# Optimization experiments

Hardware: AMD Instinct MI355X
Metric: run time of the kernel (lower is better)

## Reference

```python
import jax, jax.numpy as jnp
import numpy as np

NUM_HEADS = 16
HEAD_SIZE = 64
N_EMBD = 1024


def setup_inputs() -> dict:
    key = jax.random.key(0)
    ks = jax.random.split(key, 6)
    B, T, C = 2, 2048, N_EMBD
    scale = 0.02
    return {
        "x": jax.random.normal(ks[0], (B, T, C), dtype=jnp.float32),
        "Wq": jax.random.normal(ks[1], (C, NUM_HEADS * HEAD_SIZE), dtype=jnp.float32) * scale,
        "Wk": jax.random.normal(ks[2], (C, NUM_HEADS * HEAD_SIZE), dtype=jnp.float32) * scale,
        "Wv": jax.random.normal(ks[3], (C, NUM_HEADS * HEAD_SIZE), dtype=jnp.float32) * scale,
        "Wo": jax.random.normal(ks[4], (NUM_HEADS * HEAD_SIZE, C), dtype=jnp.float32) * scale,
        "bo": jnp.zeros((C,), dtype=jnp.float32),
    }


def reference(x, Wq, Wk, Wv, Wo, bo):
    B, T, C = x.shape
    H, D = NUM_HEADS, HEAD_SIZE
    # QKV projections (no bias), reshape to [B, H, T, D]
    q = (x @ Wq).reshape(B, T, H, D).transpose(0, 2, 1, 3)
    k = (x @ Wk).reshape(B, T, H, D).transpose(0, 2, 1, 3)
    v = (x @ Wv).reshape(B, T, H, D).transpose(0, 2, 1, 3)
    # scaled dot-product scores [B, H, T, T]
    scores = jnp.einsum("bhqd,bhkd->bhqk", q, k) / jnp.sqrt(jnp.float32(D))
    causal = jnp.tril(jnp.ones((T, T), dtype=bool))
    scores = jnp.where(causal, scores, -jnp.inf)
    weights = jax.nn.softmax(scores, axis=-1)  # dropout = identity (eval)
    out = jnp.einsum("bhqk,bhkd->bhqd", weights, v)
    out = out.transpose(0, 2, 1, 3).reshape(B, T, H * D)
    return out @ Wo + bo
```

## Files before the change

kernel.cpp:

```cpp
#include <hip/hip_runtime.h>

typedef __attribute__((ext_vector_type(8))) _Float16 f16x8;
typedef __attribute__((ext_vector_type(4))) _Float16 f16x4;
typedef __attribute__((ext_vector_type(2))) _Float16 f16x2;
typedef __attribute__((ext_vector_type(2))) __fp16   fp16x2_raw;
typedef __attribute__((ext_vector_type(4))) float    f32x4;

#define NUM_HEADS 16
#define HEAD_D 64
#define EMB 1024
#define SEQ 2048
#define BATCH 2
#define MTOT (BATCH * SEQ)

#define QALPHA 0.18033688011112042f

__device__ __forceinline__ f16x2 cvt_pk_f16(float lo, float hi)
{
    fp16x2_raw r = __builtin_amdgcn_cvt_pkrtz(lo, hi);
    return __builtin_bit_cast(f16x2, r);
}

#if defined(__has_builtin)
#if __has_builtin(__builtin_amdgcn_exp2f)
#define HAVE_EXP2 1
#endif
#endif
__device__ __forceinline__ float fast_exp2(float x)
{
#ifdef HAVE_EXP2
    return __builtin_amdgcn_exp2f(x);
#else
    return __expf(x * 0.6931471805599453f);
#endif
}

#if defined(__has_builtin)
#if __has_builtin(__builtin_amdgcn_global_load_lds)
#define HAVE_GLOAD_LDS 1
#endif
#endif

__device__ __forceinline__ void stage16(const void* g, void* ldsWaveBase, int lane)
{
#ifdef HAVE_GLOAD_LDS
    __builtin_amdgcn_global_load_lds(
        (const __attribute__((address_space(1))) void*)g,
        (__attribute__((address_space(3))) void*)ldsWaveBase, 16, 0, 0);
    (void)lane;
#else
    *(f16x8*)((char*)ldsWaveBase + lane * 16) = *(const f16x8*)g;
#endif
}

__global__ __launch_bounds__(256) void prep_all(
    const float* __restrict__ x,
    const float* __restrict__ Wq, const float* __restrict__ Wk,
    const float* __restrict__ Wv, const float* __restrict__ Wo,
    _Float16* __restrict__ xh, _Float16* __restrict__ Wt,
    _Float16* __restrict__ Wto)
{
    const int z = blockIdx.z;
    if (z == 4) {
        int base = ((blockIdx.y * 32 + blockIdx.x) * 256 + threadIdx.x) * 2;
        #pragma unroll
        for (int t = 0; t < 2; ++t) {
            int i = base + t;
            float4 a = ((const float4*)x)[i * 2];
            float4 b = ((const float4*)x)[i * 2 + 1];
            f16x8 o;
            o[0] = (_Float16)a.x; o[1] = (_Float16)a.y;
            o[2] = (_Float16)a.z; o[3] = (_Float16)a.w;
            o[4] = (_Float16)b.x; o[5] = (_Float16)b.y;
            o[6] = (_Float16)b.z; o[7] = (_Float16)b.w;
            ((f16x8*)xh)[i] = o;
        }
        return;
    }
    const float* W = z == 0 ? Wq : (z == 1 ? Wk : (z == 2 ? Wv : Wo));
    _Float16* D = (z == 3) ? Wto : (Wt + (size_t)z * EMB * EMB);
    __shared__ float tile[32][33];
    const int tx = threadIdx.x & 31, ty = threadIdx.x >> 5;
    const int n0 = blockIdx.x * 32, k0 = blockIdx.y * 32;
    #pragma unroll
    for (int j = 0; j < 4; ++j)
        tile[ty + j * 8][tx] = W[(size_t)(k0 + ty + j * 8) * EMB + n0 + tx];
    __syncthreads();
    #pragma unroll
    for (int j = 0; j < 4; ++j)
        D[(size_t)(n0 + ty + j * 8) * EMB + k0 + tx] =
            (_Float16)tile[tx][ty + j * 8];
}

__global__ __launch_bounds__(256) void gemm_qkv(
    const _Float16* __restrict__ A, const _Float16* __restrict__ Bt,
    _Float16* __restrict__ Qh, _Float16* __restrict__ Kh,
    _Float16* __restrict__ VhT)
{
    __shared__ __align__(16) _Float16 As[128 * 32];
    __shared__ __align__(16) _Float16 Bs[128 * 32];

    const int tid = threadIdx.x;
    const int w = tid >> 6, lane = tid & 63;
    const int l15 = lane & 15, g4 = lane >> 4;
    const int wm = w >> 1, wn = w & 1;

    const int wg = blockIdx.y * gridDim.x + blockIdx.x;
    const int t  = (wg & 7) * 96 + (wg >> 3);
    const int bx = t >> 5, by = t & 31;
    const int row0 = by * 128, col0 = bx * 128;

    f32x4 acc[4][4];
    #pragma unroll
    for (int mt = 0; mt < 4; ++mt)
        #pragma unroll
        for (int nt = 0; nt < 4; ++nt)
            acc[mt][nt] = (f32x4){0.f, 0.f, 0.f, 0.f};

    for (int k0 = 0; k0 < EMB; k0 += 32) {
        __syncthreads();
        #pragma unroll
        for (int i = 0; i < 2; ++i) {
            int c = (i << 8) + tid;
            int row = c >> 2, u = c & 3;
            stage16(&A[(size_t)(row0 + row) * EMB + k0 + (u << 3)],
                    (char*)As + (i << 12) + (w << 10), lane);
            stage16(&Bt[(size_t)(col0 + row) * EMB + k0 + (u << 3)],
                    (char*)Bs + (i << 12) + (w << 10), lane);
        }
        __syncthreads();

        f16x8 af[4], bf[4];
        #pragma unroll
        for (int mt = 0; mt < 4; ++mt)
            af[mt] = *(const f16x8*)((const char*)As +
                     ((wm << 6) + (mt << 4) + l15) * 64 + (g4 << 4));
        #pragma unroll
        for (int nt = 0; nt < 4; ++nt)
            bf[nt] = *(const f16x8*)((const char*)Bs +
                     ((wn << 6) + (nt << 4) + l15) * 64 + (g4 << 4));
        #pragma unroll
        for (int mt = 0; mt < 4; ++mt)
            #pragma unroll
            for (int nt = 0; nt < 4; ++nt)
                acc[mt][nt] = __builtin_amdgcn_mfma_f32_16x16x32_f16(
                    af[mt], bf[nt], acc[mt][nt], 0, 0, 0);
    }

    #pragma unroll
    for (int mt = 0; mt < 4; ++mt) {
        int m = row0 + (wm << 6) + (mt << 4) + (g4 << 2);
        #pragma unroll
        for (int nt = 0; nt < 4; ++nt) {
            int gcol = col0 + (wn << 6) + (nt << 4) + l15;
            int proj = gcol >> 10, pc = gcol & 1023;
            int h = pc >> 6, d = pc & 63;
            int b = m >> 11, tt = m & 2047;
            int bh = b * NUM_HEADS + h;
            if (proj == 2) {
                f16x4 v4;
                v4[0] = (_Float16)acc[mt][nt][0];
                v4[1] = (_Float16)acc[mt][nt][1];
                v4[2] = (_Float16)acc[mt][nt][2];
                v4[3] = (_Float16)acc[mt][nt][3];
                *(f16x4*)&VhT[((size_t)bh * HEAD_D + d) * SEQ + tt] = v4;
            } else {
                _Float16* dst = proj == 0 ? Qh : Kh;
                float alpha = proj == 0 ? QALPHA : 1.0f;
                #pragma unroll
                for (int r = 0; r < 4; ++r)
                    dst[((size_t)bh * SEQ + tt + r) * HEAD_D + d] =
                        (_Float16)(acc[mt][nt][r] * alpha);
            }
        }
    }
}

__global__ __launch_bounds__(256) void gemm_out(
    const _Float16* __restrict__ A, const _Float16* __restrict__ Bt,
    float* __restrict__ outf, const float* __restrict__ bias)
{
    __shared__ __align__(16) _Float16 As[128 * 32];
    __shared__ __align__(16) _Float16 Bs[64 * 32];

    const int tid = threadIdx.x;
    const int w = tid >> 6, lane = tid & 63;
    const int l15 = lane & 15, g4 = lane >> 4;
    const int wm = w >> 1, wn = w & 1;

    const int wg = blockIdx.y * gridDim.x + blockIdx.x;
    const int t  = (wg & 7) * 64 + (wg >> 3);
    const int bx = t >> 5, by = t & 31;
    const int row0 = by * 128, col0 = bx * 64;

    f32x4 acc[4][2];
    #pragma unroll
    for (int mt = 0; mt < 4; ++mt)
        #pragma unroll
        for (int nt = 0; nt < 2; ++nt)
            acc[mt][nt] = (f32x4){0.f, 0.f, 0.f, 0.f};

    for (int k0 = 0; k0 < EMB; k0 += 32) {
        __syncthreads();
        #pragma unroll
        for (int i = 0; i < 2; ++i) {
            int c = (i << 8) + tid;
            int row = c >> 2, u = c & 3;
            stage16(&A[(size_t)(row0 + row) * EMB + k0 + (u << 3)],
                    (char*)As + (i << 12) + (w << 10), lane);
        }
        {
            int row = tid >> 2, u = tid & 3;
            stage16(&Bt[(size_t)(col0 + row) * EMB + k0 + (u << 3)],
                    (char*)Bs + (w << 10), lane);
        }
        __syncthreads();

        f16x8 af[4], bf[2];
        #pragma unroll
        for (int mt = 0; mt < 4; ++mt)
            af[mt] = *(const f16x8*)((const char*)As +
                     ((wm << 6) + (mt << 4) + l15) * 64 + (g4 << 4));
        #pragma unroll
        for (int nt = 0; nt < 2; ++nt)
            bf[nt] = *(const f16x8*)((const char*)Bs +
                     ((wn << 5) + (nt << 4) + l15) * 64 + (g4 << 4));
        #pragma unroll
        for (int mt = 0; mt < 4; ++mt)
            #pragma unroll
            for (int nt = 0; nt < 2; ++nt)
                acc[mt][nt] = __builtin_amdgcn_mfma_f32_16x16x32_f16(
                    af[mt], bf[nt], acc[mt][nt], 0, 0, 0);
    }

    #pragma unroll
    for (int mt = 0; mt < 4; ++mt) {
        int m = row0 + (wm << 6) + (mt << 4) + (g4 << 2);
        #pragma unroll
        for (int nt = 0; nt < 2; ++nt) {
            int gcol = col0 + (wn << 5) + (nt << 4) + l15;
            float bz = bias[gcol];
            #pragma unroll
            for (int r = 0; r < 4; ++r)
                outf[(size_t)(m + r) * EMB + gcol] = acc[mt][nt][r] + bz;
        }
    }
}

__device__ __forceinline__ void stage_kv_tile(
    const _Float16* __restrict__ KhB, const _Float16* __restrict__ VtB,
    int kv0, char* __restrict__ KsBuf, char* __restrict__ VtBuf,
    int w, int lane)
{
    #pragma unroll
    for (int i = 0; i < 2; ++i) {
        int c = (i << 8) + (w << 6) + lane;
        int row = c >> 3, u = c & 7;
        int us = u ^ (row & 7);
        stage16(&KhB[(size_t)(kv0 + row) * HEAD_D + (us << 3)],
                KsBuf + (i << 12) + (w << 10), lane);
        stage16(&VtB[(size_t)row * SEQ + kv0 + (us << 3)],
                VtBuf + (i << 12) + (w << 10), lane);
    }
}

__device__ __forceinline__ void attn_tile(
    const char* __restrict__ KsC, const char* __restrict__ VtC,
    char* __restrict__ pwv,
    f16x8 qf0, f16x8 qf1, f32x4 (&acc)[4], float& m, float& l,
    bool diag, int qrel, int l15, int g)
{
    f32x4 st[4];
    #pragma unroll
    for (int nt = 0; nt < 4; ++nt) {
        int kvl = (nt << 4) + l15;
        f16x8 kf0 = *(const f16x8*)&KsC[kvl * 128 + (((g << 4)) ^ ((kvl & 7) << 4))];
        f16x8 kf1 = *(const f16x8*)&KsC[kvl * 128 + ((64 + (g << 4)) ^ ((kvl & 7) << 4))];
        f32x4 z = (f32x4){0.f, 0.f, 0.f, 0.f};
        z = __builtin_amdgcn_mfma_f32_16x16x32_f16(kf0, qf0, z, 0, 0, 0);
        z = __builtin_amdgcn_mfma_f32_16x16x32_f16(kf1, qf1, z, 0, 0, 0);
        st[nt] = z;
    }
    if (diag) {
        #pragma unroll
        for (int nt = 0; nt < 4; ++nt)
            #pragma unroll
            for (int r = 0; r < 4; ++r)
                if ((nt << 4) + (g << 2) + r > qrel) st[nt][r] = -1e30f;
    }

    float mx;
    {
        float a0 = fmaxf(fmaxf(st[0][0], st[0][1]), fmaxf(st[0][2], st[0][3]));
        float a1 = fmaxf(fmaxf(st[1][0], st[1][1]), fmaxf(st[1][2], st[1][3]));
        float a2 = fmaxf(fmaxf(st[2][0], st[2][1]), fmaxf(st[2][2], st[2][3]));
        float a3 = fmaxf(fmaxf(st[3][0], st[3][1]), fmaxf(st[3][2], st[3][3]));
        mx = fmaxf(fmaxf(a0, a1), fmaxf(a2, a3));
    }

    if (!__all(mx - m <= 8.0f)) {
        float mxr = fmaxf(mx, __shfl_xor(mx, 16));
        mxr = fmaxf(mxr, __shfl_xor(mxr, 32));
        float nm = fmaxf(m, mxr);
        float sc = fast_exp2(m - nm);
        m = nm;
        l *= sc;
        #pragma unroll
        for (int r = 0; r < 4; ++r) {
            float scr = __shfl(sc, (g << 2) + r);
            acc[0][r] *= scr; acc[1][r] *= scr;
            acc[2][r] *= scr; acc[3][r] *= scr;
        }
    }

    float ps = 0.f;
    #pragma unroll
    for (int nt = 0; nt < 4; ++nt)
        #pragma unroll
        for (int r = 0; r < 4; ++r) {
            float p = fast_exp2(st[nt][r] - m);
            st[nt][r] = p;
            ps += p;
        }
    l += ps;

    #pragma unroll
    for (int nt = 0; nt < 4; ++nt)
        #pragma unroll
        for (int rr = 0; rr < 2; ++rr) {
            int kvb = (nt << 4) + (g << 2) + (rr << 1);
            f16x2 pv = cvt_pk_f16(st[nt][rr * 2], st[nt][rr * 2 + 1]);
            *(f16x2*)&pwv[l15 * 128 + ((kvb << 1) ^ ((l15 & 7) << 4))] = pv;
        }
    f16x8 pa0 = *(const f16x8*)&pwv[l15 * 128 + (((g << 4)) ^ ((l15 & 7) << 4))];
    f16x8 pa1 = *(const f16x8*)&pwv[l15 * 128 + ((64 + (g << 4)) ^ ((l15 & 7) << 4))];

    #pragma unroll
    for (int dn = 0; dn < 4; ++dn) {
        int d = (dn << 4) + l15;
        f16x8 vf0 = *(const f16x8*)&VtC[d * 128 + (((g << 4)) ^ ((d & 7) << 4))];
        f16x8 vf1 = *(const f16x8*)&VtC[d * 128 + ((64 + (g << 4)) ^ ((d & 7) << 4))];
        acc[dn] = __builtin_amdgcn_mfma_f32_16x16x32_f16(pa0, vf0, acc[dn], 0, 0, 0);
        acc[dn] = __builtin_amdgcn_mfma_f32_16x16x32_f16(pa1, vf1, acc[dn], 0, 0, 0);
    }
}

__global__ __launch_bounds__(256) void attn_mfma(
    const _Float16* __restrict__ Qh, const _Float16* __restrict__ Kh,
    const _Float16* __restrict__ VhT, _Float16* __restrict__ O)
{
    __shared__ char lds[48 * 1024];

    const int qtA = blockIdx.x;
    const int qtB = (SEQ / 64 - 1) - qtA;
    const int bh = blockIdx.y;
    const int q0A = qtA << 6, q0B = qtB << 6;
    const int tid = threadIdx.x;
    const int w = tid >> 6, lane = tid & 63;
    const int l15 = lane & 15, g = lane >> 4;

    const _Float16* KhB = Kh  + (size_t)bh * SEQ * HEAD_D;
    const _Float16* VtB = VhT + (size_t)bh * HEAD_D * SEQ;
    const size_t headbase = (size_t)bh * SEQ * HEAD_D;

    const int qrowA = q0A + (w << 4) + l15;
    const int qrowB = q0B + (w << 4) + l15;
    f16x8 qfA0 = *(const f16x8*)&Qh[headbase + (size_t)qrowA * HEAD_D + (g << 3)];
    f16x8 qfA1 = *(const f16x8*)&Qh[headbase + (size_t)qrowA * HEAD_D + 32 + (g << 3)];
    f16x8 qfB0 = *(const f16x8*)&Qh[headbase + (size_t)qrowB * HEAD_D + (g << 3)];
    f16x8 qfB1 = *(const f16x8*)&Qh[headbase + (size_t)qrowB * HEAD_D + 32 + (g << 3)];

    f32x4 accA[4], accB[4];
    #pragma unroll
    for (int dn = 0; dn < 4; ++dn) {
        accA[dn] = (f32x4){0.f, 0.f, 0.f, 0.f};
        accB[dn] = (f32x4){0.f, 0.f, 0.f, 0.f};
    }
    float mA = -1e30f, lA = 0.f, mB = -1e30f, lB = 0.f;

    stage_kv_tile(KhB, VtB, 0, lds, lds + 16384, w, lane);
    __syncthreads();

    char* pwvA = lds + 32768 + (w << 11);
    char* pwvB = lds + 40960 + (w << 11);

    int cur = 0;
    for (int kt = 0; kt <= qtB; ++kt) {
        if (kt < qtB)
            stage_kv_tile(KhB, VtB, (kt + 1) << 6,
                          lds + ((cur ^ 1) << 13),
                          lds + 16384 + ((cur ^ 1) << 13), w, lane);

        const char* KsC = lds + (cur << 13);
        const char* VtC = lds + 16384 + (cur << 13);
        const int qrel = (w << 4) + l15;

        if (kt <= qtA) {
            attn_tile(KsC, VtC, pwvA, qfA0, qfA1, accA, mA, lA,
                      kt == qtA, qrel, l15, g);
            attn_tile(KsC, VtC, pwvB, qfB0, qfB1, accB, mB, lB,
                      false, qrel, l15, g);
        } else {
            attn_tile(KsC, VtC, pwvB, qfB0, qfB1, accB, mB, lB,
                      kt == qtB, qrel, l15, g);
        }

        __syncthreads();
        cur ^= 1;
    }

    lA += __shfl_xor(lA, 16); lA += __shfl_xor(lA, 32);
    lB += __shfl_xor(lB, 16); lB += __shfl_xor(lB, 32);
    const int b = bh >> 4, h = bh & 15;
    const float rlA = 1.f / lA, rlB = 1.f / lB;
    #pragma unroll
    for (int r = 0; r < 4; ++r) {
        float invA = __shfl(rlA, (g << 2) + r);
        float invB = __shfl(rlB, (g << 2) + r);
        int tokA = (b << 11) + q0A + (w << 4) + (g << 2) + r;
        int tokB = (b << 11) + q0B + (w << 4) + (g << 2) + r;
        #pragma unroll
        for (int dn = 0; dn < 4; ++dn) {
            O[(size_t)tokA * EMB + (h << 6) + (dn << 4) + l15] =
                (_Float16)(accA[dn][r] * invA);
            O[(size_t)tokB * EMB + (h << 6) + (dn << 4) + l15] =
                (_Float16)(accB[dn][r] * invB);
        }
    }
}

extern "C" void kernel_launch(void* const* d_in, const int* in_sizes, int n_in,
                              void* d_out, int out_size, void* d_ws, size_t ws_size,
                              hipStream_t stream)
{
    const float* x  = (const float*)d_in[0];
    const float* Wq = (const float*)d_in[1];
    const float* Wk = (const float*)d_in[2];
    const float* Wv = (const float*)d_in[3];
    const float* Wo = (const float*)d_in[4];
    const float* bo = (const float*)d_in[5];
    float* out = (float*)d_out;

    const size_t ME = (size_t)MTOT * EMB;
    const size_t WE = (size_t)EMB * EMB;
    const size_t need = (5 * ME + 4 * WE) * sizeof(_Float16);
    if (ws_size < need) return;

    _Float16* xh  = (_Float16*)d_ws;
    _Float16* Wt  = xh + ME;
    _Float16* Wto = Wt + 3 * WE;
    _Float16* Qh  = Wto + WE;
    _Float16* Kh  = Qh + ME;
    _Float16* VhT = Kh + ME;
    _Float16* Ow  = VhT + ME;

    prep_all<<<dim3(EMB / 32, EMB / 32, 5), 256, 0, stream>>>(
        x, Wq, Wk, Wv, Wo, xh, Wt, Wto);

    gemm_qkv<<<dim3(3 * EMB / 128, MTOT / 128), 256, 0, stream>>>(
        xh, Wt, Qh, Kh, VhT);

    attn_mfma<<<dim3(SEQ / 128, BATCH * NUM_HEADS), 256, 0, stream>>>(Qh, Kh, VhT, Ow);

    gemm_out<<<dim3(EMB / 64, MTOT / 128), 256, 0, stream>>>(
        Ow, Wto, out, bo);
}
```

Measured before the change: 116.7 us.

## Deepen KV prefetch to a 4-slot ring and pair tiles in B-only phase

Expands the KV LDS staging from double-buffering to a 4-slot ring with a prefetch distance of two tiles. The loop is split into three phases: a joint A/B phase, a single-tile transition step, and a B-only phase. The B-only phase uses a new attn_tile2 that computes scores for two KV tiles and does one online-softmax max/rescale per pair, halving barriers and rescale overhead there. The cost is LDS growing from 48 KB to 80 KB per block, which cuts how many blocks fit per CU. The launch_bounds hint of 4 blocks per CU cannot be met with that LDS footprint.

```diff
diff --git a/kernel.cpp b/kernel.cpp
--- a/kernel.cpp
+++ b/kernel.cpp
@@ -345,11 +345,108 @@
     }
 }
 
-__global__ __launch_bounds__(256) void attn_mfma(
+__device__ __forceinline__ void attn_tile2(
+    const char* __restrict__ Ks0, const char* __restrict__ Vt0,
+    const char* __restrict__ Ks1, const char* __restrict__ Vt1,
+    char* __restrict__ pwv,
+    f16x8 qf0, f16x8 qf1, f32x4 (&acc)[4], float& m, float& l,
+    bool diag1, int qrel, int l15, int g)
+{
+    f32x4 st[8];
+    #pragma unroll
+    for (int nt = 0; nt < 4; ++nt) {
+        int kvl = (nt << 4) + l15;
+        int off0 = kvl * 128 + (((g << 4)) ^ ((kvl & 7) << 4));
+        int off1 = kvl * 128 + ((64 + (g << 4)) ^ ((kvl & 7) << 4));
+        f16x8 ka0 = *(const f16x8*)&Ks0[off0];
+        f16x8 ka1 = *(const f16x8*)&Ks0[off1];
+        f32x4 z = (f32x4){0.f, 0.f, 0.f, 0.f};
+        z = __builtin_amdgcn_mfma_f32_16x16x32_f16(ka0, qf0, z, 0, 0, 0);
+        z = __builtin_amdgcn_mfma_f32_16x16x32_f16(ka1, qf1, z, 0, 0, 0);
+        st[nt] = z;
+        f16x8 kb0 = *(const f16x8*)&Ks1[off0];
+        f16x8 kb1 = *(const f16x8*)&Ks1[off1];
+        f32x4 z2 = (f32x4){0.f, 0.f, 0.f, 0.f};
+        z2 = __builtin_amdgcn_mfma_f32_16x16x32_f16(kb0, qf0, z2, 0, 0, 0);
+        z2 = __builtin_amdgcn_mfma_f32_16x16x32_f16(kb1, qf1, z2, 0, 0, 0);
+        st[4 + nt] = z2;
+    }
+    if (diag1) {
+        #pragma unroll
+        for (int nt = 0; nt < 4; ++nt)
+            #pragma unroll
+            for (int r = 0; r < 4; ++r)
+                if ((nt << 4) + (g << 2) + r > qrel) st[4 + nt][r] = -1e30f;
+    }
+
+    float mx;
+    {
+        float a = -1e30f;
+        #pragma unroll
+        for (int i = 0; i < 8; ++i)
+            a = fmaxf(a, fmaxf(fmaxf(st[i][0], st[i][1]),
+                               fmaxf(st[i][2], st[i][3])));
+        mx = a;
+    }
+
+    if (!__all(mx - m <= 8.0f)) {
+        float mxr = fmaxf(mx, __shfl_xor(mx, 16));
+        mxr = fmaxf(mxr, __shfl_xor(mxr, 32));
+        float nm = fmaxf(m, mxr);
+        float sc = fast_exp2(m - nm);
+        m = nm;
+        l *= sc;
+        #pragma unroll
+        for (int r = 0; r < 4; ++r) {
+            float scr = __shfl(sc, (g << 2) + r);
+            acc[0][r] *= scr; acc[1][r] *= scr;
+            acc[2][r] *= scr; acc[3][r] *= scr;
+        }
+    }
+
+    float ps = 0.f;
+    #pragma unroll
+    for (int i = 0; i < 8; ++i)
+        #pragma unroll
+        for (int r = 0; r < 4; ++r) {
+            float p = fast_exp2(st[i][r] - m);
+            st[i][r] = p;
+            ps += p;
+        }
+    l += ps;
+
+    #pragma unroll
+    for (int tile = 0; tile < 2; ++tile) {
+        const f32x4* s4 = &st[tile << 2];
+        const char* Vt = tile ? Vt1 : Vt0;
+        #pragma unroll
+        for (int nt = 0; nt < 4; ++nt)
+            #pragma unroll
+            for (int rr = 0; rr < 2; ++rr) {
+                int kvb = (nt << 4) + (g << 2) + (rr << 1);
+                f16x2 pv = cvt_pk_f16(s4[nt][rr * 2], s4[nt][rr * 2 + 1]);
+                *(f16x2*)&pwv[l15 * 128 + ((kvb << 1) ^ ((l15 & 7) << 4))] = pv;
+            }
+        f16x8 pa0 = *(const f16x8*)&pwv[l15 * 128 + (((g << 4)) ^ ((l15 & 7) << 4))];
+        f16x8 pa1 = *(const f16x8*)&pwv[l15 * 128 + ((64 + (g << 4)) ^ ((l15 & 7) << 4))];
+        #pragma unroll
+        for (int dn = 0; dn < 4; ++dn) {
+            int d = (dn << 4) + l15;
+            f16x8 vf0 = *(const f16x8*)&Vt[d * 128 + (((g << 4)) ^ ((d & 7) << 4))];
+            f16x8 vf1 = *(const f16x8*)&Vt[d * 128 + ((64 + (g << 4)) ^ ((d & 7) << 4))];
+            acc[dn] = __builtin_amdgcn_mfma_f32_16x16x32_f16(pa0, vf0, acc[dn], 0, 0, 0);
+            acc[dn] = __builtin_amdgcn_mfma_f32_16x16x32_f16(pa1, vf1, acc[dn], 0, 0, 0);
+        }
+    }
+}
+
+__global__ __launch_bounds__(256, 4) void attn_mfma(
     const _Float16* __restrict__ Qh, const _Float16* __restrict__ Kh,
     const _Float16* __restrict__ VhT, _Float16* __restrict__ O)
 {
-    __shared__ char lds[48 * 1024];
+    __shared__ char lds[80 * 1024];
+#define KSLOT(s) (lds + ((s) << 13))
+#define VSLOT(s) (lds + 32768 + ((s) << 13))
 
     const int qtA = blockIdx.x;
     const int qtB = (SEQ / 64 - 1) - qtA;
@@ -378,35 +475,46 @@
     }
     float mA = -1e30f, lA = 0.f, mB = -1e30f, lB = 0.f;
 
-    stage_kv_tile(KhB, VtB, 0, lds, lds + 16384, w, lane);
+    stage_kv_tile(KhB, VtB, 0,  KSLOT(0), VSLOT(0), w, lane);
+    stage_kv_tile(KhB, VtB, 64, KSLOT(1), VSLOT(1), w, lane);
     __syncthreads();
 
-    char* pwvA = lds + 32768 + (w << 11);
-    char* pwvB = lds + 40960 + (w << 11);
-
-    int cur = 0;
-    for (int kt = 0; kt <= qtB; ++kt) {
-        if (kt < qtB)
-            stage_kv_tile(KhB, VtB, (kt + 1) << 6,
-                          lds + ((cur ^ 1) << 13),
-                          lds + 16384 + ((cur ^ 1) << 13), w, lane);
-
-        const char* KsC = lds + (cur << 13);
-        const char* VtC = lds + 16384 + (cur << 13);
-        const int qrel = (w << 4) + l15;
-
-        if (kt <= qtA) {
-            attn_tile(KsC, VtC, pwvA, qfA0, qfA1, accA, mA, lA,
-                      kt == qtA, qrel, l15, g);
-            attn_tile(KsC, VtC, pwvB, qfB0, qfB1, accB, mB, lB,
-                      false, qrel, l15, g);
-        } else {
-            attn_tile(KsC, VtC, pwvB, qfB0, qfB1, accB, mB, lB,
-                      kt == qtB, qrel, l15, g);
-        }
-
-        __syncthreads();
-        cur ^= 1;
+    char* pwvA = lds + 65536 + (w << 11);
+    char* pwvB = lds + 73728 + (w << 11);
+    const int qrel = (w << 4) + l15;
+
+    for (int kt = 0; kt <= qtA; ++kt) {
+        int pf = kt + 2;
+        if (pf <= qtB)
+            stage_kv_tile(KhB, VtB, pf << 6, KSLOT(pf & 3), VSLOT(pf & 3), w, lane);
+        attn_tile(KSLOT(kt & 3), VSLOT(kt & 3), pwvA, qfA0, qfA1, accA, mA, lA,
+                  kt == qtA, qrel, l15, g);
+        attn_tile(KSLOT(kt & 3), VSLOT(kt & 3), pwvB, qfB0, qfB1, accB, mB, lB,
+                  false, qrel, l15, g);
+        __syncthreads();
+    }
+
+    {
+        int kt = qtA + 1;
+        int pf = kt + 2;
+        if (pf <= qtB)
+            stage_kv_tile(KhB, VtB, pf << 6, KSLOT(pf & 3), VSLOT(pf & 3), w, lane);
+        attn_tile(KSLOT(kt & 3), VSLOT(kt & 3), pwvB, qfB0, qfB1, accB, mB, lB,
+                  kt == qtB, qrel, l15, g);
+        __syncthreads();
+    }
+
+    for (int kt = qtA + 2; kt < qtB; kt += 2) {
+        int pf0 = kt + 2, pf1 = kt + 3;
+        if (pf0 <= qtB)
+            stage_kv_tile(KhB, VtB, pf0 << 6, KSLOT(pf0 & 3), VSLOT(pf0 & 3), w, lane);
+        if (pf1 <= qtB)
+            stage_kv_tile(KhB, VtB, pf1 << 6, KSLOT(pf1 & 3), VSLOT(pf1 & 3), w, lane);
+        attn_tile2(KSLOT(kt & 3), VSLOT(kt & 3),
+                   KSLOT((kt + 1) & 3), VSLOT((kt + 1) & 3),
+                   pwvB, qfB0, qfB1, accB, mB, lB,
+                   (kt + 1) == qtB, qrel, l15, g);
+        __syncthreads();
     }
 
     lA += __shfl_xor(lA, 16); lA += __shfl_xor(lA, 32);
@@ -427,6 +535,8 @@
                 (_Float16)(accB[dn][r] * invB);
         }
     }
+#undef KSLOT
+#undef VSLOT
 }
 
 extern "C" void kernel_launch(void* const* d_in, const int* in_sizes, int n_in,
```

Result: faster. 112.6 us (-3.5%).
